# Optimization experiments

Measured on AMD Instinct MI355X. Metric: run time of the kernel, lower is better.

Reference implementation:

```python
import jax, jax.numpy as jnp
import numpy as np

B, N, H = 4, 256, 128
T = 8  # triplet hidden width


def _linear_init(key, fan_in, fan_out):
    s = 1.0 / np.sqrt(fan_in)
    kw, kb = jax.random.split(key)
    W = jax.random.uniform(kw, (fan_in, fan_out), minval=-s, maxval=s, dtype=jnp.float32)
    b = jax.random.uniform(kb, (fan_out,), minval=-s, maxval=s, dtype=jnp.float32)
    return W, b


def setup_inputs() -> dict:
    key = jax.random.key(0)
    ks = jax.random.split(key, 16)
    inp = {
        "node_embeddings": jax.random.normal(ks[0], (B, N, H), dtype=jnp.float32),
        "edge_embeddings": jax.random.normal(ks[1], (B, N, H), dtype=jnp.float32),
        "graph_embeddings": jax.random.normal(ks[2], (B, H), dtype=jnp.float32),
        "previous_hidden": jax.random.normal(ks[3], (B, N, H), dtype=jnp.float32),
    }
    # message MLP: (z_i 2H, z_j 2H, edge_j H, graph H) = 6H -> H -> H -> H
    inp["Wm1"], inp["bm1"] = _linear_init(ks[4], 6 * H, H)
    inp["Wm2"], inp["bm2"] = _linear_init(ks[5], H, H)
    inp["Wm3"], inp["bm3"] = _linear_init(ks[6], H, H)
    # gate MLP: (z 2H, m H, edge H, graph H) = 5H -> H -> H (sigmoid)
    inp["Wg1"], inp["bg1"] = _linear_init(ks[7], 5 * H, H)
    inp["Wg2"], inp["bg2"] = _linear_init(ks[8], H, H)
    # readout: (z 2H, m H) = 3H -> H
    inp["Wr"], inp["br"] = _linear_init(ks[9], 3 * H, H)
    # triplet MLP: (node_j H, node_k H, node H, edge 3H, graph H) = 7H -> 8 (relu)
    inp["Wt1"], inp["bt1"] = _linear_init(ks[10], 7 * H, T)
    # triplet edge readout: 8 -> H
    inp["Wt2"], inp["bt2"] = _linear_init(ks[11], T, H)
    # layer norm params
    inp["gamma"] = jnp.ones((H,), dtype=jnp.float32)
    inp["beta"] = jnp.zeros((H,), dtype=jnp.float32)
    return inp


def reference(node_embeddings, edge_embeddings, graph_embeddings, previous_hidden,
              Wm1, bm1, Wm2, bm2, Wm3, bm3,
              Wg1, bg1, Wg2, bg2, Wr, br,
              Wt1, bt1, Wt2, bt2, gamma, beta):
    h = node_embeddings.shape[-1]
    z = jnp.concatenate([node_embeddings, previous_hidden], axis=-1)  # [B,N,2H]

    # ---- pairwise messages: decompose first linear so the 6H-wide concat is never built ----
    W_zi, W_zj = Wm1[: 2 * h], Wm1[2 * h: 4 * h]
    W_e, W_g = Wm1[4 * h: 5 * h], Wm1[5 * h:]
    u = z @ W_zi + (graph_embeddings @ W_g)[:, None, :] + bm1   # per-i part [B,N,H]
    v = z @ W_zj + edge_embeddings @ W_e                        # per-j part [B,N,H]
    h1 = jax.nn.relu(u[:, :, None, :] + v[:, None, :, :])       # [B,Ni,Nj,H]
    h2 = jax.nn.relu(h1 @ Wm2 + bm2)
    msgs = h2 @ Wm3 + bm3                                       # [B,Ni,Nj,H]
    m = jnp.max(msgs, axis=2)                                   # max over j -> [B,N,H]

    gb = jnp.broadcast_to(graph_embeddings[:, None, :], node_embeddings.shape)
    gate_in = jnp.concatenate([z, m, edge_embeddings, gb], axis=-1)  # [B,N,5H]
    g = jax.nn.sigmoid(jax.nn.relu(gate_in @ Wg1 + bg1) @ Wg2 + bg2)
    h_i = jnp.concatenate([z, m], axis=-1) @ Wr + br
    h_g = g * h_i + (1.0 - g) * previous_hidden

    # ---- triplet messages ----
    # pre-activation is separable over (j, k, i), so max over the N^2 (k,j) pairs
    # equals per-channel max_j + max_k (relu is monotone, max commutes with it).
    Wt_j, Wt_k, Wt_n = Wt1[:h], Wt1[h: 2 * h], Wt1[2 * h: 3 * h]
    Wt_e = Wt1[3 * h: 4 * h] + Wt1[4 * h: 5 * h] + Wt1[5 * h: 6 * h]
    Wt_g = Wt1[6 * h:]
    a_j = node_embeddings @ Wt_j   # [B,N,8]
    a_k = node_embeddings @ Wt_k   # [B,N,8]
    c = node_embeddings @ Wt_n + edge_embeddings @ Wt_e + (graph_embeddings @ Wt_g)[:, None, :] + bt1
    t_max = jax.nn.relu(c + jnp.max(a_j, axis=1, keepdims=True) + jnp.max(a_k, axis=1, keepdims=True))
    h_ij = t_max @ Wt2 + bt2       # [B,N,H]

    # ---- layer norm on gated hidden ----
    mu = jnp.mean(h_g, axis=-1, keepdims=True)
    var = jnp.mean(jnp.square(h_g - mu), axis=-1, keepdims=True)
    h_norm = (h_g - mu) * jax.lax.rsqrt(var + 1e-5) * gamma + beta
    return (h_norm, h_ij)
```

## Files before the change

kernel.cpp:

```cpp
#include <hip/hip_runtime.h>
#include <hip/hip_bf16.h>

typedef unsigned short u16;
typedef unsigned int u32;
typedef float f32x4 __attribute__((ext_vector_type(4)));
typedef short s16x8 __attribute__((ext_vector_type(8)));

#define MFMA16(a,b,c) __builtin_amdgcn_mfma_f32_16x16x32_bf16((a),(b),(c),0,0,0)

static __device__ __forceinline__ u16 f2bf(float x){
  union { __hip_bfloat16 b; u16 u; } c;
  c.b = __float2bfloat16(x);
  return c.u;
}

static __device__ __forceinline__ void softbar() {
  __builtin_amdgcn_sched_barrier(0);
  asm volatile("s_waitcnt lgkmcnt(0)" ::: "memory");
  __builtin_amdgcn_s_barrier();
  __builtin_amdgcn_sched_barrier(0);
}

__global__ void prep_kernel(const float* __restrict__ Wm1, const float* __restrict__ Wm2,
                            const float* __restrict__ Wm3, const float* __restrict__ Wg1,
                            const float* __restrict__ Wr,  const float* __restrict__ Wt1,
                            const float* __restrict__ node,const float* __restrict__ prev,
                            const float* __restrict__ edge,const float* __restrict__ graph,
                            u16* __restrict__ WbT, u16* __restrict__ WgrT,
                            u16* __restrict__ Wm2T, u16* __restrict__ Wm3T,
                            u16* __restrict__ gin)
{
  int idx = blockIdx.x * 256 + threadIdx.x;
  if (idx < 147456) {
    int n = idx >> 9, k = idx & 511;
    int part = k >> 7, kk = k & 127;
    float v = 0.f;
    if (n < 128) {
      if (part == 0)      v = Wm1[kk*128 + n];
      else if (part == 1) v = Wm1[(128+kk)*128 + n];
      else if (part == 3) v = Wm1[(640+kk)*128 + n];
    } else if (n < 256) {
      int nn = n - 128;
      if (part == 0)      v = Wm1[(256+kk)*128 + nn];
      else if (part == 1) v = Wm1[(384+kk)*128 + nn];
      else if (part == 2) v = Wm1[(512+kk)*128 + nn];
    } else if (n < 280) {
      int tt = n - 256;
      if (tt < 8)       { if (part == 0) v = Wt1[kk*8 + tt]; }
      else if (tt < 16) { if (part == 0) v = Wt1[(128+kk)*8 + (tt-8)]; }
      else {
        int t = tt - 16;
        if (part == 0)      v = Wt1[(256+kk)*8 + t];
        else if (part == 2) v = Wt1[(384+kk)*8 + t] + Wt1[(512+kk)*8 + t] + Wt1[(640+kk)*8 + t];
        else if (part == 3) v = Wt1[(768+kk)*8 + t];
      }
    }
    WbT[idx] = f2bf(v);
    return;
  }
  idx -= 147456;
  if (idx < 163840) {
    int n = idx / 640, k = idx - n*640;
    int part = k >> 7, kk = k & 127;
    float v = 0.f;
    if (n < 128) {
      int r = (part==0) ? kk : (part==1) ? (128+kk) : (part==2) ? (384+kk)
                        : (part==3) ? (512+kk) : (256+kk);
      v = Wg1[r*128 + n];
    } else {
      int nn = n - 128;
      if (part == 0)      v = Wr[kk*128 + nn];
      else if (part == 1) v = Wr[(128+kk)*128 + nn];
      else if (part == 4) v = Wr[(256+kk)*128 + nn];
    }
    WgrT[idx] = f2bf(v);
    return;
  }
  idx -= 163840;
  if (idx < 16384) { int n = idx >> 7, k = idx & 127; Wm2T[idx] = f2bf(Wm2[k*128 + n]); return; }
  idx -= 16384;
  if (idx < 16384) { int n = idx >> 7, k = idx & 127; Wm3T[idx] = f2bf(Wm3[k*128 + n]); return; }
  idx -= 16384;
  {
    int row = idx >> 9, k = idx & 511;
    int part = k >> 7, kk = k & 127;
    float v;
    if (part == 0)      v = node[row*128 + kk];
    else if (part == 1) v = prev[row*128 + kk];
    else if (part == 2) v = edge[row*128 + kk];
    else                v = graph[(row >> 8)*128 + kk];
    gin[row*640 + k] = f2bf(v);
  }
}

__global__ __launch_bounds__(256) void gemm_uvt_kernel(const u16* __restrict__ gin,
                                                       const u16* __restrict__ WbT,
                                                       float* __restrict__ uvt)
{
  int m0 = blockIdx.x * 16, n0 = blockIdx.y * 16;
  int tid = threadIdx.x;
  int w = tid >> 6, lane = tid & 63;
  int c = lane & 15, g = lane >> 4;
  __shared__ float cpart[4][16][17];
  const u16* arow = gin + (size_t)(m0 + c) * 640;
  const u16* brow = WbT + (size_t)(n0 + c) * 512;
  f32x4 acc = {0.f, 0.f, 0.f, 0.f};
#pragma unroll
  for (int kk = 0; kk < 4; ++kk) {
    int k0 = w*4 + kk;
    s16x8 a = *reinterpret_cast<const s16x8*>(arow + k0*32 + g*8);
    s16x8 b = *reinterpret_cast<const s16x8*>(brow + k0*32 + g*8);
    acc = MFMA16(a, b, acc);
  }
#pragma unroll
  for (int r = 0; r < 4; ++r) cpart[w][g*4 + r][c] = acc[r];
  __syncthreads();
  int row = tid >> 4, col = tid & 15;
  float s = cpart[0][row][col] + cpart[1][row][col]
          + cpart[2][row][col] + cpart[3][row][col];
  uvt[(size_t)(m0 + row) * 288 + n0 + col] = s;
}

__global__ void maxat_kernel(const float* __restrict__ uvt, float* __restrict__ mjk)
{
  int b = blockIdx.x;
  int tid = threadIdx.x;
  int row = b*256 + tid;
  __shared__ float part[4][16];
  float v[16];
#pragma unroll
  for (int t = 0; t < 16; ++t) v[t] = uvt[(size_t)row*288 + 256 + t];
#pragma unroll
  for (int off = 32; off >= 1; off >>= 1) {
#pragma unroll
    for (int t = 0; t < 16; ++t) v[t] = fmaxf(v[t], __shfl_xor(v[t], off));
  }
  int wid = tid >> 6;
  if ((tid & 63) == 0) {
#pragma unroll
    for (int t = 0; t < 16; ++t) part[wid][t] = v[t];
  }
  __syncthreads();
  if (tid < 16)
    mjk[b*16 + tid] = fmaxf(fmaxf(part[0][tid], part[1][tid]),
                            fmaxf(part[2][tid], part[3][tid]));
}

__global__ __launch_bounds__(256) void msgmax_kernel(const float* __restrict__ uvt,
    const u16* __restrict__ Wm2T, const u16* __restrict__ Wm3T,
    const float* __restrict__ bm1, const float* __restrict__ bm2,
    const float* __restrict__ bm3, u16* __restrict__ gin)
{
  const int row = blockIdx.x;
  const int b   = row >> 8;
  const int tid = threadIdx.x;
  const int w   = tid >> 6;
  const int lane = tid & 63;
  const int c = lane & 15, g = lane >> 4;

  __shared__ u16 a1s[2][4][16][40];
  __shared__ u16 h2s[2][16][136];

  s16x8 wb2[4][2], wb3[4][2];
#pragma unroll
  for (int mt = 0; mt < 2; ++mt) {
    int col = w*32 + mt*16 + c;
#pragma unroll
    for (int k0 = 0; k0 < 4; ++k0) {
      wb2[k0][mt] = *reinterpret_cast<const s16x8*>(Wm2T + col*128 + k0*32 + g*8);
      wb3[k0][mt] = *reinterpret_cast<const s16x8*>(Wm3T + col*128 + k0*32 + g*8);
    }
  }
  float4 bm2v[2];
#pragma unroll
  for (int mt = 0; mt < 2; ++mt)
    bm2v[mt] = *reinterpret_cast<const float4*>(bm2 + w*32 + mt*16 + 4*g);

  const float* urow = uvt + (size_t)row * 288;
  float uf[8];
  {
    int off = w*32 + g*8;
    float4 x = *reinterpret_cast<const float4*>(urow + off);
    float4 y = *reinterpret_cast<const float4*>(urow + off + 4);
    float4 p = *reinterpret_cast<const float4*>(bm1 + off);
    float4 q = *reinterpret_cast<const float4*>(bm1 + off + 4);
    uf[0]=x.x+p.x; uf[1]=x.y+p.y; uf[2]=x.z+p.z; uf[3]=x.w+p.w;
    uf[4]=y.x+q.x; uf[5]=y.y+q.y; uf[6]=y.z+q.z; uf[7]=y.w+q.w;
  }

  const float* vb = uvt + (size_t)(b*256) * 288 + 128;
  f32x4 mmax[2];
#pragma unroll
  for (int mt = 0; mt < 2; ++mt)
#pragma unroll
    for (int r = 0; r < 4; ++r) mmax[mt][r] = -1e30f;

  float4 vc[2][2];
#define LOADV(IT) do { \
  _Pragma("unroll") \
  for (int t = 0; t < 2; ++t) { \
    const float* p_ = vb + (size_t)((IT)*32 + t*16 + c) * 288 + w*32 + g*8; \
    vc[t][0] = *reinterpret_cast<const float4*>(p_); \
    vc[t][1] = *reinterpret_cast<const float4*>(p_ + 4); } } while (0)

  LOADV(0);

  for (int it = 0; it < 8; ++it) {
#pragma unroll
    for (int t = 0; t < 2; ++t) {
      u32 d0 = (u32)f2bf(fmaxf(uf[0] + vc[t][0].x, 0.f))
             | ((u32)f2bf(fmaxf(uf[1] + vc[t][0].y, 0.f)) << 16);
      u32 d1 = (u32)f2bf(fmaxf(uf[2] + vc[t][0].z, 0.f))
             | ((u32)f2bf(fmaxf(uf[3] + vc[t][0].w, 0.f)) << 16);
      u32 d2 = (u32)f2bf(fmaxf(uf[4] + vc[t][1].x, 0.f))
             | ((u32)f2bf(fmaxf(uf[5] + vc[t][1].y, 0.f)) << 16);
      u32 d3 = (u32)f2bf(fmaxf(uf[6] + vc[t][1].z, 0.f))
             | ((u32)f2bf(fmaxf(uf[7] + vc[t][1].w, 0.f)) << 16);
      uint4 pk = {d0, d1, d2, d3};
      *reinterpret_cast<uint4*>(&a1s[t][w][c][g*8]) = pk;
    }
    if (it < 7) LOADV(it + 1);
    softbar();

    f32x4 acc1[2][2] = {{{0,0,0,0},{0,0,0,0}},{{0,0,0,0},{0,0,0,0}}};
#pragma unroll
    for (int t = 0; t < 2; ++t)
#pragma unroll
      for (int k0 = 0; k0 < 4; ++k0) {
        s16x8 af = *reinterpret_cast<const s16x8*>(&a1s[t][k0][c][g*8]);
        acc1[t][0] = MFMA16(wb2[k0][0], af, acc1[t][0]);
        acc1[t][1] = MFMA16(wb2[k0][1], af, acc1[t][1]);
      }

#pragma unroll
    for (int t = 0; t < 2; ++t)
#pragma unroll
      for (int mt = 0; mt < 2; ++mt) {
        u32 lo = (u32)f2bf(fmaxf(acc1[t][mt][0] + bm2v[mt].x, 0.f))
               | ((u32)f2bf(fmaxf(acc1[t][mt][1] + bm2v[mt].y, 0.f)) << 16);
        u32 hi = (u32)f2bf(fmaxf(acc1[t][mt][2] + bm2v[mt].z, 0.f))
               | ((u32)f2bf(fmaxf(acc1[t][mt][3] + bm2v[mt].w, 0.f)) << 16);
        uint2 pk = {lo, hi};
        *reinterpret_cast<uint2*>(&h2s[t][c][w*32 + mt*16 + 4*g]) = pk;
      }
    softbar();

    f32x4 acc2[2][2] = {{{0,0,0,0},{0,0,0,0}},{{0,0,0,0},{0,0,0,0}}};
#pragma unroll
    for (int t = 0; t < 2; ++t)
#pragma unroll
      for (int k0 = 0; k0 < 4; ++k0) {
        s16x8 a2 = *reinterpret_cast<const s16x8*>(&h2s[t][c][k0*32 + g*8]);
        acc2[t][0] = MFMA16(wb3[k0][0], a2, acc2[t][0]);
        acc2[t][1] = MFMA16(wb3[k0][1], a2, acc2[t][1]);
      }
#pragma unroll
    for (int mt = 0; mt < 2; ++mt)
#pragma unroll
      for (int r = 0; r < 4; ++r)
        mmax[mt][r] = fmaxf(mmax[mt][r], fmaxf(acc2[0][mt][r], acc2[1][mt][r]));
  }
#undef LOADV

#pragma unroll
  for (int mt = 0; mt < 2; ++mt) {
    f32x4 m = mmax[mt];
#pragma unroll
    for (int off = 1; off < 16; off <<= 1) {
      m[0] = fmaxf(m[0], __shfl_xor(m[0], off));
      m[1] = fmaxf(m[1], __shfl_xor(m[1], off));
      m[2] = fmaxf(m[2], __shfl_xor(m[2], off));
      m[3] = fmaxf(m[3], __shfl_xor(m[3], off));
    }
    if (c == 0) {
      int col = w*32 + mt*16 + 4*g;
      u32 lo = (u32)f2bf(m[0] + bm3[col])   | ((u32)f2bf(m[1] + bm3[col+1]) << 16);
      u32 hi = (u32)f2bf(m[2] + bm3[col+2]) | ((u32)f2bf(m[3] + bm3[col+3]) << 16);
      uint2 pk = {lo, hi};
      *reinterpret_cast<uint2*>(gin + (size_t)row*640 + 512 + col) = pk;
    }
  }
}

__global__ __launch_bounds__(256) void gemm_gate_kernel(const u16* __restrict__ gin,
                                 const u16* __restrict__ WgrT,
                                 const float* __restrict__ bg1, const float* __restrict__ br,
                                 float* __restrict__ r1, float* __restrict__ hi)
{
  int m0 = blockIdx.x * 16, n0 = blockIdx.y * 16;
  int tid = threadIdx.x;
  int w = tid >> 6, lane = tid & 63;
  int c = lane & 15, g = lane >> 4;
  __shared__ float cpart[4][16][17];
  const u16* arow = gin  + (size_t)(m0 + c) * 640;
  const u16* brow = WgrT + (size_t)(n0 + c) * 640;
  f32x4 acc = {0.f, 0.f, 0.f, 0.f};
#pragma unroll
  for (int kk = 0; kk < 5; ++kk) {
    int k0 = w*5 + kk;
    s16x8 a = *reinterpret_cast<const s16x8*>(arow + k0*32 + g*8);
    s16x8 b = *reinterpret_cast<const s16x8*>(brow + k0*32 + g*8);
    acc = MFMA16(a, b, acc);
  }
#pragma unroll
  for (int r = 0; r < 4; ++r) cpart[w][g*4 + r][c] = acc[r];
  __syncthreads();
  int row = tid >> 4, col = tid & 15;
  float s = cpart[0][row][col] + cpart[1][row][col]
          + cpart[2][row][col] + cpart[3][row][col];
  int coln = n0 + col;
  int gr = m0 + row;
  if (coln < 128) r1[gr*128 + coln] = fmaxf(s + bg1[coln], 0.f);
  else            hi[gr*128 + coln - 128] = s + br[coln - 128];
}

__global__ void finalize_kernel(const float* __restrict__ r1, const float* __restrict__ hi,
                                const float* __restrict__ prev, const float* __restrict__ uvt,
                                const float* __restrict__ mjk,
                                const float* __restrict__ Wg2, const float* __restrict__ bg2,
                                const float* __restrict__ bt1, const float* __restrict__ Wt2,
                                const float* __restrict__ bt2, const float* __restrict__ gamma,
                                const float* __restrict__ beta, float* __restrict__ out)
{
  int row = blockIdx.x;
  int h = threadIdx.x;
  int b = row >> 8;
  __shared__ float r1s[128];
  __shared__ float red[4];
  r1s[h] = r1[row*128 + h];
  __syncthreads();
  float glin = bg2[h];
#pragma unroll 8
  for (int k = 0; k < 128; ++k) glin += r1s[k] * Wg2[k*128 + h];
  float g = 1.f / (1.f + __expf(-glin));
  float hg = g * hi[row*128 + h] + (1.f - g) * prev[row*128 + h];

  float s1 = hg, s2 = hg*hg;
#pragma unroll
  for (int off = 1; off < 64; off <<= 1) {
    s1 += __shfl_xor(s1, off);
    s2 += __shfl_xor(s2, off);
  }
  int wid = h >> 6;
  if ((h & 63) == 0) { red[wid] = s1; red[2 + wid] = s2; }
  __syncthreads();
  float mu  = (red[0] + red[1]) * 0.0078125f;
  float ex2 = (red[2] + red[3]) * 0.0078125f;
  float var = ex2 - mu*mu;
  float hn = (hg - mu) * rsqrtf(var + 1e-5f) * gamma[h] + beta[h];
  out[row*128 + h] = hn;

  float o2 = bt2[h];
#pragma unroll
  for (int t = 0; t < 8; ++t) {
    float tv = uvt[(size_t)row*288 + 272 + t] + bt1[t] + mjk[b*16 + t] + mjk[b*16 + 8 + t];
    tv = fmaxf(tv, 0.f);
    o2 += tv * Wt2[t*128 + h];
  }
  out[131072 + row*128 + h] = o2;
}

extern "C" void kernel_launch(void* const* d_in, const int* in_sizes, int n_in,
                              void* d_out, int out_size, void* d_ws, size_t ws_size,
                              hipStream_t stream) {
  const float* node  = (const float*)d_in[0];
  const float* edge  = (const float*)d_in[1];
  const float* graph = (const float*)d_in[2];
  const float* prev  = (const float*)d_in[3];
  const float* Wm1 = (const float*)d_in[4];
  const float* bm1 = (const float*)d_in[5];
  const float* Wm2 = (const float*)d_in[6];
  const float* bm2 = (const float*)d_in[7];
  const float* Wm3 = (const float*)d_in[8];
  const float* bm3 = (const float*)d_in[9];
  const float* Wg1 = (const float*)d_in[10];
  const float* bg1 = (const float*)d_in[11];
  const float* Wg2 = (const float*)d_in[12];
  const float* bg2 = (const float*)d_in[13];
  const float* Wr  = (const float*)d_in[14];
  const float* br  = (const float*)d_in[15];
  const float* Wt1 = (const float*)d_in[16];
  const float* bt1 = (const float*)d_in[17];
  const float* Wt2 = (const float*)d_in[18];
  const float* bt2 = (const float*)d_in[19];
  const float* gamma = (const float*)d_in[20];
  const float* beta  = (const float*)d_in[21];
  float* out = (float*)d_out;

  char* ws = (char*)d_ws;
  u16*   WbT  = (u16*)(ws + 0);
  u16*   WgrT = (u16*)(ws + 294912);
  u16*   Wm2T = (u16*)(ws + 622592);
  u16*   Wm3T = (u16*)(ws + 655360);
  u16*   gin  = (u16*)(ws + 688128);
  float* uvt  = (float*)(ws + 1998848);
  float* r1   = (float*)(ws + 3178496);
  float* hi   = (float*)(ws + 3702784);
  float* mjk  = (float*)(ws + 4227072);

  prep_kernel<<<3392, 256, 0, stream>>>(Wm1, Wm2, Wm3, Wg1, Wr, Wt1,
                                        node, prev, edge, graph,
                                        WbT, WgrT, Wm2T, Wm3T, gin);
  gemm_uvt_kernel<<<dim3(64, 18), 256, 0, stream>>>(gin, WbT, uvt);
  maxat_kernel<<<4, 256, 0, stream>>>(uvt, mjk);
  msgmax_kernel<<<1024, 256, 0, stream>>>(uvt, Wm2T, Wm3T, bm1, bm2, bm3, gin);
  gemm_gate_kernel<<<dim3(64, 16), 256, 0, stream>>>(gin, WgrT, bg1, br, r1, hi);
  finalize_kernel<<<1024, 128, 0, stream>>>(r1, hi, prev, uvt, mjk,
                                            Wg2, bg2, bt1, Wt2, bt2, gamma, beta, out);
}
```

Baseline: 61.28 us.

## Split message max over j into two halves and merge in gate GEMM

```diff
diff --git a/kernel.cpp b/kernel.cpp
--- a/kernel.cpp
+++ b/kernel.cpp
@@ -149,9 +149,11 @@
 __global__ __launch_bounds__(256) void msgmax_kernel(const float* __restrict__ uvt,
     const u16* __restrict__ Wm2T, const u16* __restrict__ Wm3T,
     const float* __restrict__ bm1, const float* __restrict__ bm2,
-    const float* __restrict__ bm3, u16* __restrict__ gin)
-{
-  const int row = blockIdx.x;
+    float* __restrict__ pmax)
+{
+  const int bx  = blockIdx.x;
+  const int row = bx >> 1;
+  const int jh  = bx & 1;
   const int b   = row >> 8;
   const int tid = threadIdx.x;
   const int w   = tid >> 6;
@@ -199,13 +201,13 @@
 #define LOADV(IT) do { \
   _Pragma("unroll") \
   for (int t = 0; t < 2; ++t) { \
-    const float* p_ = vb + (size_t)((IT)*32 + t*16 + c) * 288 + w*32 + g*8; \
+    const float* p_ = vb + (size_t)(jh*128 + (IT)*32 + t*16 + c) * 288 + w*32 + g*8; \
     vc[t][0] = *reinterpret_cast<const float4*>(p_); \
     vc[t][1] = *reinterpret_cast<const float4*>(p_ + 4); } } while (0)
 
   LOADV(0);
 
-  for (int it = 0; it < 8; ++it) {
+  for (int it = 0; it < 4; ++it) {
 #pragma unroll
     for (int t = 0; t < 2; ++t) {
       u32 d0 = (u32)f2bf(fmaxf(uf[0] + vc[t][0].x, 0.f))
@@ -219,7 +221,7 @@
       uint4 pk = {d0, d1, d2, d3};
       *reinterpret_cast<uint4*>(&a1s[t][w][c][g*8]) = pk;
     }
-    if (it < 7) LOADV(it + 1);
+    if (it < 3) LOADV(it + 1);
     softbar();
 
     f32x4 acc1[2][2] = {{{0,0,0,0},{0,0,0,0}},{{0,0,0,0},{0,0,0,0}}};
@@ -274,16 +276,15 @@
     }
     if (c == 0) {
       int col = w*32 + mt*16 + 4*g;
-      u32 lo = (u32)f2bf(m[0] + bm3[col])   | ((u32)f2bf(m[1] + bm3[col+1]) << 16);
-      u32 hi = (u32)f2bf(m[2] + bm3[col+2]) | ((u32)f2bf(m[3] + bm3[col+3]) << 16);
-      uint2 pk = {lo, hi};
-      *reinterpret_cast<uint2*>(gin + (size_t)row*640 + 512 + col) = pk;
+      float4 o = {m[0], m[1], m[2], m[3]};
+      *reinterpret_cast<float4*>(pmax + (size_t)row*256 + jh*128 + col) = o;
     }
   }
 }
 
 __global__ __launch_bounds__(256) void gemm_gate_kernel(const u16* __restrict__ gin,
                                  const u16* __restrict__ WgrT,
+                                 const float* __restrict__ pmax, const float* __restrict__ bm3,
                                  const float* __restrict__ bg1, const float* __restrict__ br,
                                  float* __restrict__ r1, float* __restrict__ hi)
 {
@@ -292,13 +293,35 @@
   int w = tid >> 6, lane = tid & 63;
   int c = lane & 15, g = lane >> 4;
   __shared__ float cpart[4][16][17];
+  __shared__ u16 ms[16][136];
+
+  {
+    int rr = tid & 15, cb = (tid >> 4) * 8;
+    const float* pr = pmax + (size_t)(m0 + rr) * 256;
+    float4 a0 = *reinterpret_cast<const float4*>(pr + cb);
+    float4 a1 = *reinterpret_cast<const float4*>(pr + cb + 4);
+    float4 b0 = *reinterpret_cast<const float4*>(pr + 128 + cb);
+    float4 b1 = *reinterpret_cast<const float4*>(pr + 128 + cb + 4);
+    float4 t0 = *reinterpret_cast<const float4*>(bm3 + cb);
+    float4 t1 = *reinterpret_cast<const float4*>(bm3 + cb + 4);
+    u32 d0 = (u32)f2bf(fmaxf(a0.x,b0.x)+t0.x) | ((u32)f2bf(fmaxf(a0.y,b0.y)+t0.y) << 16);
+    u32 d1 = (u32)f2bf(fmaxf(a0.z,b0.z)+t0.z) | ((u32)f2bf(fmaxf(a0.w,b0.w)+t0.w) << 16);
+    u32 d2 = (u32)f2bf(fmaxf(a1.x,b1.x)+t1.x) | ((u32)f2bf(fmaxf(a1.y,b1.y)+t1.y) << 16);
+    u32 d3 = (u32)f2bf(fmaxf(a1.z,b1.z)+t1.z) | ((u32)f2bf(fmaxf(a1.w,b1.w)+t1.w) << 16);
+    uint4 pk = {d0, d1, d2, d3};
+    *reinterpret_cast<uint4*>(&ms[rr][cb]) = pk;
+  }
+  __syncthreads();
+
   const u16* arow = gin  + (size_t)(m0 + c) * 640;
   const u16* brow = WgrT + (size_t)(n0 + c) * 640;
   f32x4 acc = {0.f, 0.f, 0.f, 0.f};
 #pragma unroll
   for (int kk = 0; kk < 5; ++kk) {
     int k0 = w*5 + kk;
-    s16x8 a = *reinterpret_cast<const s16x8*>(arow + k0*32 + g*8);
+    s16x8 a;
+    if (k0 < 16) a = *reinterpret_cast<const s16x8*>(arow + k0*32 + g*8);
+    else         a = *reinterpret_cast<const s16x8*>(&ms[c][(k0-16)*32 + g*8]);
     s16x8 b = *reinterpret_cast<const s16x8*>(brow + k0*32 + g*8);
     acc = MFMA16(a, b, acc);
   }
@@ -397,14 +420,16 @@
   float* r1   = (float*)(ws + 3178496);
   float* hi   = (float*)(ws + 3702784);
   float* mjk  = (float*)(ws + 4227072);
+  float* pmax = (float*)(ws + 4227584);
 
   prep_kernel<<<3392, 256, 0, stream>>>(Wm1, Wm2, Wm3, Wg1, Wr, Wt1,
                                         node, prev, edge, graph,
                                         WbT, WgrT, Wm2T, Wm3T, gin);
   gemm_uvt_kernel<<<dim3(64, 18), 256, 0, stream>>>(gin, WbT, uvt);
   maxat_kernel<<<4, 256, 0, stream>>>(uvt, mjk);
-  msgmax_kernel<<<1024, 256, 0, stream>>>(uvt, Wm2T, Wm3T, bm1, bm2, bm3, gin);
-  gemm_gate_kernel<<<dim3(64, 16), 256, 0, stream>>>(gin, WgrT, bg1, br, r1, hi);
+  msgmax_kernel<<<2048, 256, 0, stream>>>(uvt, Wm2T, Wm3T, bm1, bm2, pmax);
+  gemm_gate_kernel<<<dim3(64, 16), 256, 0, stream>>>(gin, WgrT, pmax, bm3,
+                                                     bg1, br, r1, hi);
   finalize_kernel<<<1024, 128, 0, stream>>>(r1, hi, prev, uvt, mjk,
                                             Wg2, bg2, bt1, Wt2, bt2, gamma, beta, out);
 }
```

Measured after the change: 71.75 us. 17.1% more time.

## Split msgmax warps into producer/consumer pipeline with double-buffered hidden tile

Applied to the files above, without the earlier changes.

```diff
diff --git a/kernel.cpp b/kernel.cpp
--- a/kernel.cpp
+++ b/kernel.cpp
@@ -12,6 +12,9 @@
   union { __hip_bfloat16 b; u16 u; } c;
   c.b = __float2bfloat16(x);
   return c.u;
+}
+static __device__ __forceinline__ u32 pk2(float a, float b){
+  return (u32)f2bf(a) | ((u32)f2bf(b) << 16);
 }
 
 static __device__ __forceinline__ void softbar() {
@@ -157,127 +160,123 @@
   const int w   = tid >> 6;
   const int lane = tid & 63;
   const int c = lane & 15, g = lane >> 4;
-
-  __shared__ u16 a1s[2][4][16][40];
-  __shared__ u16 h2s[2][16][136];
-
-  s16x8 wb2[4][2], wb3[4][2];
-#pragma unroll
-  for (int mt = 0; mt < 2; ++mt) {
-    int col = w*32 + mt*16 + c;
+  const bool prod = (w < 2);
+  const int colbase = (w & 1) * 64;
+
+  __shared__ u16 h2s[2][32][136];
+
+  const u16* Wsel = prod ? Wm2T : Wm3T;
+  s16x8 wb[4][4];
+#pragma unroll
+  for (int mt = 0; mt < 4; ++mt) {
+    int col = colbase + mt*16 + c;
+#pragma unroll
+    for (int k0 = 0; k0 < 4; ++k0)
+      wb[k0][mt] = *reinterpret_cast<const s16x8*>(Wsel + col*128 + k0*32 + g*8);
+  }
+
+  const f32x4 z4 = {0.f, 0.f, 0.f, 0.f};
+  f32x4 uf[4][2];
+  f32x4 bm2v[4];
+  if (prod) {
+    const float* urow = uvt + (size_t)row * 288;
 #pragma unroll
     for (int k0 = 0; k0 < 4; ++k0) {
-      wb2[k0][mt] = *reinterpret_cast<const s16x8*>(Wm2T + col*128 + k0*32 + g*8);
-      wb3[k0][mt] = *reinterpret_cast<const s16x8*>(Wm3T + col*128 + k0*32 + g*8);
+      int off = k0*32 + g*8;
+      uf[k0][0] = *reinterpret_cast<const f32x4*>(urow + off)
+                + *reinterpret_cast<const f32x4*>(bm1 + off);
+      uf[k0][1] = *reinterpret_cast<const f32x4*>(urow + off + 4)
+                + *reinterpret_cast<const f32x4*>(bm1 + off + 4);
     }
-  }
-  float4 bm2v[2];
-#pragma unroll
-  for (int mt = 0; mt < 2; ++mt)
-    bm2v[mt] = *reinterpret_cast<const float4*>(bm2 + w*32 + mt*16 + 4*g);
-
-  const float* urow = uvt + (size_t)row * 288;
-  float uf[8];
-  {
-    int off = w*32 + g*8;
-    float4 x = *reinterpret_cast<const float4*>(urow + off);
-    float4 y = *reinterpret_cast<const float4*>(urow + off + 4);
-    float4 p = *reinterpret_cast<const float4*>(bm1 + off);
-    float4 q = *reinterpret_cast<const float4*>(bm1 + off + 4);
-    uf[0]=x.x+p.x; uf[1]=x.y+p.y; uf[2]=x.z+p.z; uf[3]=x.w+p.w;
-    uf[4]=y.x+q.x; uf[5]=y.y+q.y; uf[6]=y.z+q.z; uf[7]=y.w+q.w;
-  }
+#pragma unroll
+    for (int mt = 0; mt < 4; ++mt)
+      bm2v[mt] = *reinterpret_cast<const f32x4*>(bm2 + colbase + mt*16 + 4*g);
+  }
+  f32x4 mmax[4];
+#pragma unroll
+  for (int mt = 0; mt < 4; ++mt) mmax[mt] = {-1e30f, -1e30f, -1e30f, -1e30f};
 
   const float* vb = uvt + (size_t)(b*256) * 288 + 128;
-  f32x4 mmax[2];
-#pragma unroll
-  for (int mt = 0; mt < 2; ++mt)
-#pragma unroll
-    for (int r = 0; r < 4; ++r) mmax[mt][r] = -1e30f;
-
-  float4 vc[2][2];
-#define LOADV(IT) do { \
-  _Pragma("unroll") \
-  for (int t = 0; t < 2; ++t) { \
-    const float* p_ = vb + (size_t)((IT)*32 + t*16 + c) * 288 + w*32 + g*8; \
-    vc[t][0] = *reinterpret_cast<const float4*>(p_); \
-    vc[t][1] = *reinterpret_cast<const float4*>(p_ + 4); } } while (0)
-
-  LOADV(0);
-
-  for (int it = 0; it < 8; ++it) {
-#pragma unroll
-    for (int t = 0; t < 2; ++t) {
-      u32 d0 = (u32)f2bf(fmaxf(uf[0] + vc[t][0].x, 0.f))
-             | ((u32)f2bf(fmaxf(uf[1] + vc[t][0].y, 0.f)) << 16);
-      u32 d1 = (u32)f2bf(fmaxf(uf[2] + vc[t][0].z, 0.f))
-             | ((u32)f2bf(fmaxf(uf[3] + vc[t][0].w, 0.f)) << 16);
-      u32 d2 = (u32)f2bf(fmaxf(uf[4] + vc[t][1].x, 0.f))
-             | ((u32)f2bf(fmaxf(uf[5] + vc[t][1].y, 0.f)) << 16);
-      u32 d3 = (u32)f2bf(fmaxf(uf[6] + vc[t][1].z, 0.f))
-             | ((u32)f2bf(fmaxf(uf[7] + vc[t][1].w, 0.f)) << 16);
-      uint4 pk = {d0, d1, d2, d3};
-      *reinterpret_cast<uint4*>(&a1s[t][w][c][g*8]) = pk;
+
+  for (int s = 0; s <= 8; ++s) {
+    if (prod) {
+      if (s < 8) {
+        const int buf = s & 1;
+#pragma unroll
+        for (int t = 0; t < 2; ++t) {
+          const float* vrow = vb + (size_t)(s*32 + t*16 + c) * 288;
+          s16x8 a1f[4];
+#pragma unroll
+          for (int k0 = 0; k0 < 4; ++k0) {
+            int off = k0*32 + g*8;
+            f32x4 lo = __builtin_elementwise_max(
+                         *reinterpret_cast<const f32x4*>(vrow + off) + uf[k0][0], z4);
+            f32x4 hi = __builtin_elementwise_max(
+                         *reinterpret_cast<const f32x4*>(vrow + off + 4) + uf[k0][1], z4);
+            s16x8 f;
+            f[0] = (short)f2bf(lo[0]); f[1] = (short)f2bf(lo[1]);
+            f[2] = (short)f2bf(lo[2]); f[3] = (short)f2bf(lo[3]);
+            f[4] = (short)f2bf(hi[0]); f[5] = (short)f2bf(hi[1]);
+            f[6] = (short)f2bf(hi[2]); f[7] = (short)f2bf(hi[3]);
+            a1f[k0] = f;
+          }
+          f32x4 acc1[4];
+#pragma unroll
+          for (int mt = 0; mt < 4; ++mt) acc1[mt] = bm2v[mt];
+#pragma unroll
+          for (int k0 = 0; k0 < 4; ++k0)
+#pragma unroll
+            for (int mt = 0; mt < 4; ++mt)
+              acc1[mt] = MFMA16(wb[k0][mt], a1f[k0], acc1[mt]);
+#pragma unroll
+          for (int mt = 0; mt < 4; ++mt) {
+            f32x4 tv = __builtin_elementwise_max(acc1[mt], z4);
+            uint2 pk = {pk2(tv[0], tv[1]), pk2(tv[2], tv[3])};
+            *reinterpret_cast<uint2*>(&h2s[buf][t*16 + c][colbase + mt*16 + 4*g]) = pk;
+          }
+        }
+      }
+    } else {
+      if (s > 0) {
+        const int buf = (s - 1) & 1;
+#pragma unroll
+        for (int t = 0; t < 2; ++t) {
+          s16x8 a2[4];
+#pragma unroll
+          for (int k0 = 0; k0 < 4; ++k0)
+            a2[k0] = *reinterpret_cast<const s16x8*>(&h2s[buf][t*16 + c][k0*32 + g*8]);
+          f32x4 acc2[4] = {z4, z4, z4, z4};
+#pragma unroll
+          for (int k0 = 0; k0 < 4; ++k0)
+#pragma unroll
+            for (int mt = 0; mt < 4; ++mt)
+              acc2[mt] = MFMA16(wb[k0][mt], a2[k0], acc2[mt]);
+#pragma unroll
+          for (int mt = 0; mt < 4; ++mt)
+            mmax[mt] = __builtin_elementwise_max(mmax[mt], acc2[mt]);
+        }
+      }
     }
-    if (it < 7) LOADV(it + 1);
     softbar();
-
-    f32x4 acc1[2][2] = {{{0,0,0,0},{0,0,0,0}},{{0,0,0,0},{0,0,0,0}}};
-#pragma unroll
-    for (int t = 0; t < 2; ++t)
-#pragma unroll
-      for (int k0 = 0; k0 < 4; ++k0) {
-        s16x8 af = *reinterpret_cast<const s16x8*>(&a1s[t][k0][c][g*8]);
-        acc1[t][0] = MFMA16(wb2[k0][0], af, acc1[t][0]);
-        acc1[t][1] = MFMA16(wb2[k0][1], af, acc1[t][1]);
+  }
+
+  if (!prod) {
+#pragma unroll
+    for (int mt = 0; mt < 4; ++mt) {
+      f32x4 m = mmax[mt];
+#pragma unroll
+      for (int off = 1; off < 16; off <<= 1) {
+        m[0] = fmaxf(m[0], __shfl_xor(m[0], off));
+        m[1] = fmaxf(m[1], __shfl_xor(m[1], off));
+        m[2] = fmaxf(m[2], __shfl_xor(m[2], off));
+        m[3] = fmaxf(m[3], __shfl_xor(m[3], off));
       }
-
-#pragma unroll
-    for (int t = 0; t < 2; ++t)
-#pragma unroll
-      for (int mt = 0; mt < 2; ++mt) {
-        u32 lo = (u32)f2bf(fmaxf(acc1[t][mt][0] + bm2v[mt].x, 0.f))
-               | ((u32)f2bf(fmaxf(acc1[t][mt][1] + bm2v[mt].y, 0.f)) << 16);
-        u32 hi = (u32)f2bf(fmaxf(acc1[t][mt][2] + bm2v[mt].z, 0.f))
-               | ((u32)f2bf(fmaxf(acc1[t][mt][3] + bm2v[mt].w, 0.f)) << 16);
-        uint2 pk = {lo, hi};
-        *reinterpret_cast<uint2*>(&h2s[t][c][w*32 + mt*16 + 4*g]) = pk;
+      if (c == 0) {
+        int col = colbase + mt*16 + 4*g;
+        float4 b3 = *reinterpret_cast<const float4*>(bm3 + col);
+        uint2 pk = {pk2(m[0] + b3.x, m[1] + b3.y), pk2(m[2] + b3.z, m[3] + b3.w)};
+        *reinterpret_cast<uint2*>(gin + (size_t)row*640 + 512 + col) = pk;
       }
-    softbar();
-
-    f32x4 acc2[2][2] = {{{0,0,0,0},{0,0,0,0}},{{0,0,0,0},{0,0,0,0}}};
-#pragma unroll
-    for (int t = 0; t < 2; ++t)
-#pragma unroll
-      for (int k0 = 0; k0 < 4; ++k0) {
-        s16x8 a2 = *reinterpret_cast<const s16x8*>(&h2s[t][c][k0*32 + g*8]);
-        acc2[t][0] = MFMA16(wb3[k0][0], a2, acc2[t][0]);
-        acc2[t][1] = MFMA16(wb3[k0][1], a2, acc2[t][1]);
-      }
-#pragma unroll
-    for (int mt = 0; mt < 2; ++mt)
-#pragma unroll
-      for (int r = 0; r < 4; ++r)
-        mmax[mt][r] = fmaxf(mmax[mt][r], fmaxf(acc2[0][mt][r], acc2[1][mt][r]));
-  }
-#undef LOADV
-
-#pragma unroll
-  for (int mt = 0; mt < 2; ++mt) {
-    f32x4 m = mmax[mt];
-#pragma unroll
-    for (int off = 1; off < 16; off <<= 1) {
-      m[0] = fmaxf(m[0], __shfl_xor(m[0], off));
-      m[1] = fmaxf(m[1], __shfl_xor(m[1], off));
-      m[2] = fmaxf(m[2], __shfl_xor(m[2], off));
-      m[3] = fmaxf(m[3], __shfl_xor(m[3], off));
-    }
-    if (c == 0) {
-      int col = w*32 + mt*16 + 4*g;
-      u32 lo = (u32)f2bf(m[0] + bm3[col])   | ((u32)f2bf(m[1] + bm3[col+1]) << 16);
-      u32 hi = (u32)f2bf(m[2] + bm3[col+2]) | ((u32)f2bf(m[3] + bm3[col+3]) << 16);
-      uint2 pk = {lo, hi};
-      *reinterpret_cast<uint2*>(gin + (size_t)row*640 + 512 + col) = pk;
     }
   }
 }
```

Measured after the change: 79.24 us. 1.29x slower.
